# Kernel tuning notes

Measured on AMD Instinct MI355X. Metric: run time of the kernel, lower is better.

## Reference

```python
import jax, jax.numpy as jnp
import numpy as np

N_COARSE = 24
N_FINE = 1000
TOTAL_NODES = N_COARSE + N_FINE  # 1024
BATCH = 32768


def _build_state_space():
    # Faithful port of generateStateSpace for levels==2.
    # hierarchy: fine node (N_COARSE + i) has parent coarse node (i % N_COARSE),
    # fine nodes visited in order so every coarse row is inserted on first sight.
    S = np.zeros((TOTAL_NODES + 1, TOTAL_NODES), dtype=np.float32)
    recorded = np.zeros(TOTAL_NODES, dtype=np.int64)
    i = 1
    for f in range(N_FINE):
        fine = N_COARSE + f
        coarse = f % N_COARSE
        if recorded[coarse] == 0:
            S[i, coarse] = 1.0
            recorded[coarse] = 1
            i += 1
        S[i, coarse] = 1.0
        S[i, fine] = 1.0
        i += 1
    assert i == TOTAL_NODES + 1, 'Invalid StateSpace'
    return jnp.asarray(S)


def setup_inputs() -> dict:
    key = jax.random.key(0)
    k_fs, k_lab = jax.random.split(key)
    fs = jax.random.normal(k_fs, (BATCH, TOTAL_NODES), dtype=jnp.float32)
    labels = jax.random.randint(k_lab, (BATCH,), 0, TOTAL_NODES)
    stateSpace = _build_state_space()  # [TOTAL_NODES+1, TOTAL_NODES]
    return {'fs': fs, 'labels': labels, 'stateSpace': stateSpace}


def reference(fs, labels, stateSpace):
    # joint[s, b] = exp(sum_n stateSpace[s, n] * fs[b, n])
    joint = jnp.exp(jnp.einsum('sn,bn->sb', stateSpace, fs))  # [S, B]
    z = jnp.sum(joint, axis=0)                                # [B]
    # selector: states s that contain label[b] (stateSpace[s, label_b] > 0)
    sel = stateSpace[:, labels] > 0                           # [S, B]
    marginal = jnp.sum(jnp.where(sel, joint, 0.0), axis=0)    # [B]
    loss = -(jnp.log(marginal) - jnp.log(z))                  # = -log(marginal / z)
    return jnp.mean(loss)
```

## Files before the change

### kernel.cpp

```cpp
#include <hip/hip_runtime.h>
#include <hip/hip_bf16.h>


constexpr int N_COARSE = 24;
constexpr int TOTAL = 1024;
constexpr int BATCH = 32768;
constexpr int WAVES_PER_BLOCK = 4;
constexpr int GRID1 = BATCH / WAVES_PER_BLOCK;

__global__ __launch_bounds__(256) void treeloss_partial(
    const float* __restrict__ fs, const int* __restrict__ labels,
    float* __restrict__ partials) {
  const int wave = threadIdx.x >> 6;
  const int lane = threadIdx.x & 63;
  const int b = blockIdx.x * WAVES_PER_BLOCK + wave;

  __shared__ float sc[WAVES_PER_BLOCK][N_COARSE];
  __shared__ float blocksum[WAVES_PER_BLOCK];

  const float* __restrict__ row = fs + (size_t)b * TOTAL;
  const int label = labels[b];

  if (lane < N_COARSE) sc[wave][lane] = __expf(row[lane]);
  __syncthreads();

  float zp = 0.0f;
  float sp = 0.0f;
#pragma unroll
  for (int j = 0; j < 4; ++j) {
    const int n0 = j * 256 + lane * 4;
    const float4 v = *reinterpret_cast<const float4*>(row + n0);
    const float vv[4] = {v.x, v.y, v.z, v.w};
#pragma unroll
    for (int k = 0; k < 4; ++k) {
      const int n = n0 + k;
      const float en = __expf(vv[k]);
      if (j == 0 && n < N_COARSE) {
        zp += en;
        if (n == label) sp += en;
      } else {
        const int c = n % N_COARSE;
        const float t = sc[wave][c] * en;
        zp += t;
        if (n == label || c == label) sp += t;
      }
    }
  }

#pragma unroll
  for (int off = 32; off > 0; off >>= 1) {
    zp += __shfl_down(zp, off);
    sp += __shfl_down(sp, off);
  }

  if (lane == 0) {
    const float z = 1.0f + zp;
    blocksum[wave] = logf(z) - logf(sp);
  }
  __syncthreads();

  if (threadIdx.x == 0) {
    partials[blockIdx.x] = blocksum[0] + blocksum[1] + blocksum[2] + blocksum[3];
  }
}

__global__ __launch_bounds__(256) void treeloss_reduce(
    const float* __restrict__ partials, float* __restrict__ out) {
  const int lane = threadIdx.x & 63;
  const int wave = threadIdx.x >> 6;
  float s = 0.0f;
#pragma unroll
  for (int i = 0; i < GRID1 / 256; ++i)
    s += partials[threadIdx.x + i * 256];
#pragma unroll
  for (int off = 32; off > 0; off >>= 1) s += __shfl_down(s, off);
  __shared__ float ps[WAVES_PER_BLOCK];
  if (lane == 0) ps[wave] = s;
  __syncthreads();
  if (threadIdx.x == 0)
    out[0] = (ps[0] + ps[1] + ps[2] + ps[3]) * (1.0f / (float)BATCH);
}

extern "C" void kernel_launch(void* const* d_in, const int* in_sizes, int n_in,
                              void* d_out, int out_size, void* d_ws, size_t ws_size,
                              hipStream_t stream) {
  const float* fs = (const float*)d_in[0];
  const int* labels = (const int*)d_in[1];
  float* out = (float*)d_out;
  float* partials = (float*)d_ws;

  treeloss_partial<<<GRID1, 256, 0, stream>>>(fs, labels, partials);
  treeloss_reduce<<<1, 256, 0, stream>>>(partials, out);
}
```

Baseline: 191.6 us.

## Compute marginal analytically and issue all row loads before the coarse-exp barrier

The per-element label selector and its second reduction are replaced by a closed-form marginal. For a coarse label it is exp(coarse) times one plus the sum of its fine children, gathered by a strided load. For a fine label it is exp(coarse)*exp(fine). Coarse exponentials are duplicated into a 48-entry shared array so each lane indexes with a precomputed base instead of a per-element modulo. The four float4 row loads are issued before the barrier so they overlap it. The reduce kernel now uses 1024 threads with float4 loads. The extra gather for coarse labels adds scattered reads, and fast __logf slightly changes precision.

```diff
diff --git a/kernel.cpp b/kernel.cpp
--- a/kernel.cpp
+++ b/kernel.cpp
@@ -15,47 +15,74 @@
   const int lane = threadIdx.x & 63;
   const int b = blockIdx.x * WAVES_PER_BLOCK + wave;
 
-  __shared__ float sc[WAVES_PER_BLOCK][N_COARSE];
+  __shared__ float sc48[WAVES_PER_BLOCK][48];
   __shared__ float blocksum[WAVES_PER_BLOCK];
 
   const float* __restrict__ row = fs + (size_t)b * TOTAL;
+  const float4* __restrict__ row4 = reinterpret_cast<const float4*>(row);
   const int label = labels[b];
 
-  if (lane < N_COARSE) sc[wave][lane] = __expf(row[lane]);
+  const float4 v0 = row4[lane];
+  const float4 v1 = row4[lane + 64];
+  const float4 v2 = row4[lane + 128];
+  const float4 v3 = row4[lane + 192];
+
+  if (lane < N_COARSE) {
+    const float e = __expf(row[lane]);
+    sc48[wave][lane] = e;
+    sc48[wave][lane + N_COARSE] = e;
+  }
   __syncthreads();
 
+  const int cbase = (lane * 4) % N_COARSE;
   float zp = 0.0f;
-  float sp = 0.0f;
-#pragma unroll
-  for (int j = 0; j < 4; ++j) {
-    const int n0 = j * 256 + lane * 4;
-    const float4 v = *reinterpret_cast<const float4*>(row + n0);
-    const float vv[4] = {v.x, v.y, v.z, v.w};
+
+  {
+    const float vv[4] = {v0.x, v0.y, v0.z, v0.w};
 #pragma unroll
     for (int k = 0; k < 4; ++k) {
-      const int n = n0 + k;
+      const int n = lane * 4 + k;
       const float en = __expf(vv[k]);
-      if (j == 0 && n < N_COARSE) {
-        zp += en;
-        if (n == label) sp += en;
-      } else {
-        const int c = n % N_COARSE;
-        const float t = sc[wave][c] * en;
-        zp += t;
-        if (n == label || c == label) sp += t;
-      }
+      if (n < N_COARSE) zp += en;
+      else zp += sc48[wave][cbase + k] * en;
     }
+  }
+  {
+    const float vv[4] = {v1.x, v1.y, v1.z, v1.w};
+#pragma unroll
+    for (int k = 0; k < 4; ++k)
+      zp += sc48[wave][cbase + 16 + k] * __expf(vv[k]);
+  }
+  {
+    const float vv[4] = {v2.x, v2.y, v2.z, v2.w};
+#pragma unroll
+    for (int k = 0; k < 4; ++k)
+      zp += sc48[wave][cbase + 8 + k] * __expf(vv[k]);
+  }
+  {
+    const float vv[4] = {v3.x, v3.y, v3.z, v3.w};
+#pragma unroll
+    for (int k = 0; k < 4; ++k)
+      zp += sc48[wave][cbase + k] * __expf(vv[k]);
+  }
+
+  float g = 0.0f;
+  if (label < N_COARSE) {
+    const int idx = label + N_COARSE * (lane + 1);
+    if (idx < TOTAL) g = __expf(row[idx]);
   }
 
 #pragma unroll
   for (int off = 32; off > 0; off >>= 1) {
     zp += __shfl_down(zp, off);
-    sp += __shfl_down(sp, off);
+    g += __shfl_down(g, off);
   }
 
   if (lane == 0) {
-    const float z = 1.0f + zp;
-    blocksum[wave] = logf(z) - logf(sp);
+    float m;
+    if (label < N_COARSE) m = sc48[wave][label] * (1.0f + g);
+    else m = sc48[wave][label % N_COARSE] * __expf(row[label]);
+    blocksum[wave] = __logf(1.0f + zp) - __logf(m);
   }
   __syncthreads();
 
@@ -64,21 +91,26 @@
   }
 }
 
-__global__ __launch_bounds__(256) void treeloss_reduce(
+__global__ __launch_bounds__(1024) void treeloss_reduce(
     const float* __restrict__ partials, float* __restrict__ out) {
-  const int lane = threadIdx.x & 63;
-  const int wave = threadIdx.x >> 6;
-  float s = 0.0f;
-#pragma unroll
-  for (int i = 0; i < GRID1 / 256; ++i)
-    s += partials[threadIdx.x + i * 256];
+  const int tid = threadIdx.x;
+  const int lane = tid & 63;
+  const int wave = tid >> 6;
+  const float4* __restrict__ p4 = reinterpret_cast<const float4*>(partials);
+  const float4 a = p4[tid];
+  const float4 c = p4[tid + 1024];
+  float s = (a.x + a.y + a.z + a.w) + (c.x + c.y + c.z + c.w);
 #pragma unroll
   for (int off = 32; off > 0; off >>= 1) s += __shfl_down(s, off);
-  __shared__ float ps[WAVES_PER_BLOCK];
+  __shared__ float ps[16];
   if (lane == 0) ps[wave] = s;
   __syncthreads();
-  if (threadIdx.x == 0)
-    out[0] = (ps[0] + ps[1] + ps[2] + ps[3]) * (1.0f / (float)BATCH);
+  if (tid == 0) {
+    float t = 0.0f;
+#pragma unroll
+    for (int w = 0; w < 16; ++w) t += ps[w];
+    out[0] = t * (1.0f / (float)BATCH);
+  }
 }
 
 extern "C" void kernel_launch(void* const* d_in, const int* in_sizes, int n_in,
@@ -90,5 +122,5 @@
   float* partials = (float*)d_ws;
 
   treeloss_partial<<<GRID1, 256, 0, stream>>>(fs, labels, partials);
-  treeloss_reduce<<<1, 256, 0, stream>>>(partials, out);
+  treeloss_reduce<<<1, 1024, 0, stream>>>(partials, out);
 }
```

Measured after the change: 189.8 us (median of 2 runs). Within noise of the previous version (-0.9%).
